# Optimization experiments

Measured on AMD Instinct MI355X. Metric: run time of the kernel, lower is better.

## Reference

```python
import jax, jax.numpy as jnp
import numpy as np
import math

D = 768
H = 12
HD = D // H  # 64


def setup_inputs() -> dict:
    key = jax.random.key(0)
    ks = jax.random.split(key, 8)
    B, S = 32, 127
    desc = jax.random.normal(ks[0], (B, S, D), dtype=jnp.float32)
    nv = jax.random.normal(ks[1], (B, S + 1, D), dtype=jnp.float32)
    def xavier(k, shape):
        fan_in, fan_out = shape[1], shape[0]
        gain = 1.0 / math.sqrt(2.0)
        limit = gain * math.sqrt(6.0 / (fan_in + fan_out))
        return jax.random.uniform(k, shape, jnp.float32, -limit, limit)
    Wq = xavier(ks[2], (D, D)); bq = jnp.zeros((D,), jnp.float32)
    Wk = xavier(ks[3], (D, D)); bk = jnp.zeros((D,), jnp.float32)
    Wv = xavier(ks[4], (D, D)); bv = jnp.zeros((D,), jnp.float32)
    # attn_proj: Linear(3*head_dim, 1)
    Wa = xavier(ks[5], (1, 3 * HD))[0]  # [3*HD]
    ba = jnp.zeros((), jnp.float32)
    return {
        "desc_embeddings": desc,
        "name_value_embeddings": nv,
        "Wq": Wq, "bq": bq, "Wk": Wk, "bk": bk, "Wv": Wv, "bv": bv,
        "Wa": Wa, "ba": ba,
    }


def _forward(desc_embeddings, name_value_embeddings, Wq, bq, Wk, bk, Wv, bv, Wa, ba):
    B, new_seq, _ = name_value_embeddings.shape
    S = new_seq - 1

    # adjacency: var-var all ones, CLS->Var row = 1, Var->CLS col = 0, CLS->CLS = 0
    adj = jnp.zeros((new_seq, new_seq), jnp.float32)
    adj = adj.at[1:, 1:].set(1.0)
    adj = adj.at[0, 1:].set(1.0)
    adj = jnp.broadcast_to(adj, (B, new_seq, new_seq))

    # q,k,v: [B, H, new_seq, HD]
    def proj(W, b):
        y = name_value_embeddings @ W.T + b
        return y.reshape(B, new_seq, H, HD).transpose(0, 2, 1, 3)
    q = proj(Wq, bq); k = proj(Wk, bk); v = proj(Wv, bv)

    # attn_proj weight split: [q_part | k_part | edge_part], each [HD]
    wq_a, wk_a, we_a = Wa[:HD], Wa[HD:2 * HD], Wa[2 * HD:]

    # q/k scalar contributions per (b,h,i) and (b,h,j)
    lq = jnp.einsum('bhid,d->bhi', q, wq_a)  # [B,H,new_seq]
    lk = jnp.einsum('bhjd,d->bhj', k, wk_a)  # [B,H,new_seq]

    # edge_attr[b,i,j] per head h (head slice of concat[node_i_desc, node_j_desc]):
    # edge vector = concat(desc_i, desc_j)[h*HD:(h+1)*HD] viewed as [H, HD] of 2D dims.
    # concat(desc_i, desc_j) has 2D dims -> reshaped to [H, HD] means head h takes
    # slice [h*HD:(h+1)*HD] of the 2D-dim concat. Heads 0..H/2-1 come from desc_i,
    # heads H/2..H-1 come from desc_j. Compute edge dot with we_a accordingly.
    # desc_full[b,t] : [B,S,D]. Build per-head contributions:
    # for h < H//2: edge slice = desc_i[h*HD:(h+1)*HD]  -> depends only on i
    # for h >= H//2: edge slice = desc_j[(h-H//2)*HD:(h-H//2+1)*HD] -> depends only on j
    desc_heads = desc_embeddings.reshape(B, S, H // 2, 2 * HD)  # wrong split; do directly
    # Direct: per head h, slice indices into the 2D concat vector
    dh = desc_embeddings.reshape(B, S, H, HD)  # desc split into H chunks of HD (covers D = H*HD)
    # concat(desc_i,desc_j) reshaped to [H,HD]: heads 0..H/2-1 use dh_i[:, :, h],
    # heads H/2..H-1 use dh_j[:, :, h - H/2]
    e_dot = jnp.einsum('bshd,d->bsh', dh, jnp.broadcast_to(we_a, (HD,)))  # placeholder, recompute per head below
    # per-head edge scalar contribution for var-var edges:
    ei = jnp.einsum('bshd,d->bhs', dh, we_a)  # contribution if head slice comes from desc at position s
    Hh = H // 2
    # var-var logits edge part: for h<Hh depends on i; for h>=Hh depends on j
    le_i = ei[:, :Hh, :]   # [B,Hh,S] depends on i (row)
    le_j = ei[:, Hh:, :]   # [B,Hh,S] depends on j (col)

    # CLS edges: cls_edge_attr = concat(desc, desc) at position t (the var index)
    # row 0 (CLS->var j): edge = concat(desc_j, desc_j) -> head h slice:
    #   h<Hh: dh_j[h]; h>=Hh: dh_j[h-Hh]  -> scalar ei[b,h,j] with h mapped
    e_cls = jnp.concatenate([ei[:, :Hh, :], ei[:, :Hh, :]], axis=1) * 0  # init
    e_cls = jnp.concatenate([le_i, le_i], axis=1)  # [B,H,S]: head h<Hh uses dh[h], h>=Hh uses dh[h-Hh]
    # note ei[:, :Hh] corresponds to dh chunks 0..Hh-1 ; for h>=Hh slice is dh[h-Hh] -> same le_i

    # Assemble full logits [B,H,new_seq,new_seq]
    logits = lq[:, :, :, None] + lk[:, :, None, :]
    # edge contributions (only where adj==1; edge_attr zeroed elsewhere by mask mult)
    edge = jnp.zeros((B, H, new_seq, new_seq), jnp.float32)
    # var-var block [1:,1:]
    ev = jnp.zeros((B, H, S, S), jnp.float32)
    ev = ev + jnp.pad(le_i, ((0, 0), (0, Hh), (0, 0)))[:, :, :, None] * 0  # keep shapes
    ev_i = jnp.concatenate([le_i, jnp.zeros_like(le_j)], axis=1)  # h<Hh: i-dependent
    ev_j = jnp.concatenate([jnp.zeros_like(le_i), le_j], axis=1)  # h>=Hh: j-dependent
    ev = ev_i[:, :, :, None] + ev_j[:, :, None, :]  # [B,H,S,S]
    edge = edge.at[:, :, 1:, 1:].set(ev)
    # CLS row (0, 1:): cls_edge = concat(desc_j,desc_j); j = column var
    edge = edge.at[:, :, 0, 1:].set(e_cls)
    # CLS col (1:, 0): cls_edge = concat(desc_i,desc_i) BUT adj[:,1:,0]=0 so edge_attr
    # multiplied by adj -> zero; also masked out. edge stays 0, but torch zeroes it too.
    # mask edge by adjacency (edge_attr *= adj)
    edge = edge * adj[:, None, :, :]
    logits = logits + edge + ba

    mask = (adj[:, None, :, :] == 0).astype(jnp.float32) * -1e9
    logits = logits + mask
    attn = jax.nn.softmax(logits, axis=-1)  # [B,H,new_seq,new_seq]
    ctx = jnp.einsum('bhij,bhjd->bhid', attn, v)
    basis_outputs = ctx.transpose(0, 2, 1, 3)  # [B,new_seq,H,HD]
    return basis_outputs, attn


def reference(desc_embeddings, name_value_embeddings, Wq, bq, Wk, bk, Wv, bv, Wa, ba):
    return _forward(desc_embeddings, name_value_embeddings, Wq, bq, Wk, bk, Wv, bv, Wa, ba)
```

## Files before the change

kernel.cpp:

```cpp
#include <hip/hip_runtime.h>

#define NB 32
#define NS 128
#define SD 127
#define ND 768
#define NH 12
#define HD 64

__device__ inline float wredSum(float v){
  #pragma unroll
  for (int off=32; off>0; off>>=1) v += __shfl_xor(v, off);
  return v;
}
__device__ inline float wredMax(float v){
  #pragma unroll
  for (int off=32; off>0; off>>=1) v = fmaxf(v, __shfl_xor(v, off));
  return v;
}

__global__ __launch_bounds__(256)
void fold_ei(const float* __restrict__ Wk, const float* __restrict__ bk,
             const float* __restrict__ desc, const float* __restrict__ Wa,
             float* __restrict__ uk, float* __restrict__ bkdot,
             float* __restrict__ ei){
  int blk = blockIdx.x, t = threadIdx.x;
  int wave = t >> 6, lane = t & 63;
  if (blk < 144){
    __shared__ float red[4][64];
    int h = blk/12, cb = blk%12;
    int c0 = t & 63, dg = t >> 6;
    const float* base = Wk + (size_t)(h*HD + dg*16)*ND + cb*64 + c0;
    float acc = 0.f;
    #pragma unroll
    for (int i=0;i<16;++i) acc += base[(size_t)i*ND] * Wa[64 + dg*16 + i];
    red[dg][c0] = acc;
    __syncthreads();
    if (dg==0) uk[h*ND + cb*64 + c0] = red[0][c0]+red[1][c0]+red[2][c0]+red[3][c0];
    if (blk==0 && t < NH){
      float a = 0.f;
      for (int d=0; d<64; ++d) a += bk[t*HD+d]*Wa[64+d];
      bkdot[t] = a;
    }
  } else {
    int bs = blk - 144;
    int b = bs / SD, s = bs % SD;
    float wea = Wa[128 + lane];
    const float* row = desc + (size_t)bs * ND;
    #pragma unroll
    for (int hh=0; hh<3; ++hh){
      int h = wave + hh*4;
      float v = row[h*HD + lane] * wea;
      v = wredSum(v);
      if (lane==0) ei[(size_t)(b*NH + h)*NS + s] = v;
    }
  }
}

__global__ __launch_bounds__(256)
void lk_kernel(const float* __restrict__ nv, const float* __restrict__ uk,
               const float* __restrict__ bkdot, float* __restrict__ lk){
  __shared__ __align__(16) float S[4*ND];
  int blk = blockIdx.x, t = threadIdx.x, wave = t>>6, lane = t&63;
  float ukr[3][12], bkd[3];
  #pragma unroll
  for (int hh=0; hh<3; ++hh){
    int h = wave*3 + hh;
    bkd[hh] = bkdot[h];
    #pragma unroll
    for (int k=0;k<12;++k) ukr[hh][k] = uk[h*ND + lane + 64*k];
  }
  int j0 = blk*4;
  const float4* src = (const float4*)(nv + (size_t)j0*ND);
  ((float4*)S)[t]     = src[t];
  ((float4*)S)[t+256] = src[t+256];
  ((float4*)S)[t+512] = src[t+512];
  __syncthreads();
  float acc[12];
  #pragma unroll
  for (int rr=0; rr<4; ++rr)
    #pragma unroll
    for (int hh=0; hh<3; ++hh){
      float a = 0.f;
      #pragma unroll
      for (int k=0;k<12;++k) a += S[rr*ND + lane + 64*k]*ukr[hh][k];
      acc[rr*3+hh] = a;
    }
  #pragma unroll
  for (int i=0;i<12;++i) acc[i] = wredSum(acc[i]);
  if (lane == 0){
    int b = j0 >> 7, jb = j0 & 127;
    #pragma unroll
    for (int rr=0; rr<4; ++rr)
      #pragma unroll
      for (int hh=0; hh<3; ++hh)
        lk[(size_t)(b*NH + wave*3 + hh)*NS + jb + rr] = acc[rr*3+hh] + bkd[hh];
  }
}

__global__ __launch_bounds__(256)
void msoft_attn(const float* __restrict__ nv, const float* __restrict__ lk,
                const float* __restrict__ ei, float* __restrict__ m_part,
                float* __restrict__ out){
  int blk = blockIdx.x;
  int b = blk >> 4, jg = blk & 15;
  int t = threadIdx.x, wave = t >> 6, lane = t & 63;
  __shared__ float slk[NH*NS];
  __shared__ float sei[NH*NS];
  __shared__ float wf[24][NS];
  for (int i=t; i<NH*NS; i+=256) slk[i] = lk[(size_t)b*NH*NS + i];
  for (int i=t; i<NH*NS; i+=256) sei[i] = ei[(size_t)b*NH*NS + i];
  __syncthreads();
  #pragma unroll
  for (int rr=0; rr<6; ++rr){
    int r = wave*6 + rr;
    int h = r >> 1, which = r & 1;
    const float* eirow = (which==0) ? (sei + (h%6)*NS) : (sei + h*NS);
    float g = (which==0) ? 1.f : (h>=6 ? 1.f : 0.f);
    float x0 = (lane>=1) ? slk[h*NS+lane] + g*eirow[lane-1] : -3.0e38f;
    float x1 = slk[h*NS+lane+64] + g*eirow[lane+63];
    float mm = wredMax(fmaxf(x0,x1));
    float e0 = (lane>=1) ? __expf(x0-mm) : 0.f;
    float e1 = __expf(x1-mm);
    float s  = wredSum(e0+e1);
    float inv = 1.f/s;
    wf[r][lane]    = e0*inv;
    wf[r][lane+64] = e1*inv;
  }
  __syncthreads();
  if (t < 192){
    const float4* nvb = (const float4*)(nv + ((size_t)b*NS + jg*8)*ND);
    float4 acc[24];
    #pragma unroll
    for (int r=0;r<24;++r) acc[r] = make_float4(0.f,0.f,0.f,0.f);
    #pragma unroll
    for (int jj=0; jj<8; ++jj){
      float4 x = nvb[jj*192 + t];
      int j = jg*8 + jj;
      #pragma unroll
      for (int r=0;r<24;++r){
        float wr = wf[r][j];
        acc[r].x += wr*x.x; acc[r].y += wr*x.y;
        acc[r].z += wr*x.z; acc[r].w += wr*x.w;
      }
    }
    #pragma unroll
    for (int r=0;r<24;++r)
      ((float4*)(m_part + ((size_t)(b*24 + r)*16 + jg)*ND))[t] = acc[r];
  }
  float* abase = out + (size_t)NB*NS*ND + (size_t)(b*NH)*NS*NS;
  for (int idx=t; idx<3072; idx+=256){
    int h = idx >> 8;
    int rem = idx & 255;
    int il = rem >> 5, q = rem & 31;
    int i = jg*8 + il;
    const float* srcw = (i==0) ? wf[h*2] : wf[h*2+1];
    float4 v = { srcw[q*4], srcw[q*4+1], srcw[q*4+2], srcw[q*4+3] };
    ((float4*)(abase + (size_t)h*NS*NS))[i*32 + q] = v;
  }
}

__global__ __launch_bounds__(256)
void proj_basis(const float* __restrict__ m_part, const float* __restrict__ Wv,
                const float* __restrict__ bv, float* __restrict__ out){
  int bh = blockIdx.x;
  int b = bh / NH, h = bh % NH;
  int t = threadIdx.x, wave = t >> 6, lane = t & 63;
  __shared__ __align__(16) float msum[2*ND];
  __shared__ float cvec[2*HD];
  for (int i=t; i<384; i+=256){
    int rl = (i >= 192);
    int c4 = i - rl*192;
    const float4* mp = (const float4*)(m_part + ((size_t)(b*24 + h*2 + rl)*16)*ND) + c4;
    float4 s = make_float4(0.f,0.f,0.f,0.f);
    #pragma unroll
    for (int g=0; g<16; ++g){
      float4 v = mp[g*192];
      s.x += v.x; s.y += v.y; s.z += v.z; s.w += v.w;
    }
    ((float4*)msum)[i] = s;
  }
  __syncthreads();
  #pragma unroll
  for (int dd=0; dd<16; ++dd){
    int d = wave*16 + dd;
    const float* wvr = Wv + (size_t)(h*HD + d)*ND;
    float p0=0.f, p1=0.f;
    #pragma unroll
    for (int k=0; k<12; ++k){
      float wv = wvr[lane + 64*k];
      p0 += wv*msum[lane + 64*k];
      p1 += wv*msum[ND + lane + 64*k];
    }
    p0 = wredSum(p0); p1 = wredSum(p1);
    if (lane==0){
      float bb = bv[h*HD + d];
      cvec[d]    = p0 + bb;
      cvec[64+d] = p1 + bb;
    }
  }
  __syncthreads();
  float* bo = out + (size_t)b*NS*ND + h*HD;
  #pragma unroll
  for (int k=0;k<8;++k){
    int idx = t + k*256;
    int i = idx>>4, q = idx&15;
    const float* srcc = (i==0) ? cvec : cvec+64;
    float4 v = { srcc[q*4], srcc[q*4+1], srcc[q*4+2], srcc[q*4+3] };
    *(float4*)(bo + (size_t)i*ND + q*4) = v;
  }
}

extern "C" void kernel_launch(void* const* d_in, const int* in_sizes, int n_in,
                              void* d_out, int out_size, void* d_ws, size_t ws_size,
                              hipStream_t stream) {
  const float* desc = (const float*)d_in[0];
  const float* nv   = (const float*)d_in[1];
  const float* Wk   = (const float*)d_in[4];
  const float* bk   = (const float*)d_in[5];
  const float* Wv   = (const float*)d_in[6];
  const float* bv   = (const float*)d_in[7];
  const float* Wa   = (const float*)d_in[8];
  float* out = (float*)d_out;
  float* ws  = (float*)d_ws;

  float* uk     = ws;
  float* bkdot  = ws + 9216;
  float* eibuf  = ws + 9232;
  float* lkbuf  = ws + 58384;
  float* m_part = ws + 107536;

  fold_ei   <<<4208, 256, 0, stream>>>(Wk, bk, desc, Wa, uk, bkdot, eibuf);
  lk_kernel <<<1024, 256, 0, stream>>>(nv, uk, bkdot, lkbuf);
  msoft_attn<<<512,  256, 0, stream>>>(nv, lkbuf, eibuf, m_part, out);
  proj_basis<<<384,  256, 0, stream>>>(m_part, Wv, bv, out);
}
```

Before: 140.2 us.

## Fuse softmax-weighted sum and Wv projection into one per-(batch,head) kernel

Merges msoft_attn and proj_basis into a single kernel with one block per (batch, head). Each block computes its two softmax rows, reduces nv over all positions into shared memory, writes the attention map, then projects through the head's Wv slice. This removes the m_part partial-sum buffer round trip and one launch. Block order is swizzled so concurrent blocks share a batch's nv in cache. The cost is that each block streams the full nv batch (128x768 floats) using only 192 threads, so per-block serial work and nv re-reads across heads go up.

```diff
diff --git a/kernel.cpp b/kernel.cpp
--- a/kernel.cpp
+++ b/kernel.cpp
@@ -98,115 +98,98 @@
 }
 
 __global__ __launch_bounds__(256)
-void msoft_attn(const float* __restrict__ nv, const float* __restrict__ lk,
-                const float* __restrict__ ei, float* __restrict__ m_part,
-                float* __restrict__ out){
-  int blk = blockIdx.x;
-  int b = blk >> 4, jg = blk & 15;
+void attn_fused(const float* __restrict__ nv, const float* __restrict__ lk,
+                const float* __restrict__ ei, const float* __restrict__ Wv,
+                const float* __restrict__ bv, float* __restrict__ out){
+  int logical = ((blockIdx.x & 7) * 48) + (blockIdx.x >> 3);
+  int b = logical / NH, h = logical % NH;
   int t = threadIdx.x, wave = t >> 6, lane = t & 63;
-  __shared__ float slk[NH*NS];
-  __shared__ float sei[NH*NS];
-  __shared__ float wf[24][NS];
-  for (int i=t; i<NH*NS; i+=256) slk[i] = lk[(size_t)b*NH*NS + i];
-  for (int i=t; i<NH*NS; i+=256) sei[i] = ei[(size_t)b*NH*NS + i];
-  __syncthreads();
-  #pragma unroll
-  for (int rr=0; rr<6; ++rr){
-    int r = wave*6 + rr;
-    int h = r >> 1, which = r & 1;
-    const float* eirow = (which==0) ? (sei + (h%6)*NS) : (sei + h*NS);
-    float g = (which==0) ? 1.f : (h>=6 ? 1.f : 0.f);
-    float x0 = (lane>=1) ? slk[h*NS+lane] + g*eirow[lane-1] : -3.0e38f;
-    float x1 = slk[h*NS+lane+64] + g*eirow[lane+63];
+  __shared__ __align__(16) float slk[NS];
+  __shared__ __align__(16) float sei0[NS];
+  __shared__ __align__(16) float sei1[NS];
+  __shared__ __align__(16) float wf0[NS];
+  __shared__ __align__(16) float wf1[NS];
+  __shared__ __align__(16) float msum0[ND];
+  __shared__ __align__(16) float msum1[ND];
+  __shared__ __align__(16) float cvec0[HD];
+  __shared__ __align__(16) float cvec1[HD];
+
+  if (t < NS) slk[t] = lk[(size_t)(b*NH + h)*NS + t];
+  if (t < SD) sei0[t] = ei[(size_t)(b*NH + (h % 6))*NS + t];
+  if (t >= 128 && t < 128 + SD) sei1[t-128] = ei[(size_t)(b*NH + h)*NS + (t-128)];
+  __syncthreads();
+
+  if (wave < 2){
+    const float* eir = (wave==0) ? sei0 : sei1;
+    float g = (wave==0) ? 1.f : (h >= 6 ? 1.f : 0.f);
+    float x0 = (lane>=1) ? slk[lane] + g*eir[lane-1] : -3.0e38f;
+    float x1 = slk[lane+64] + g*eir[lane+63];
     float mm = wredMax(fmaxf(x0,x1));
     float e0 = (lane>=1) ? __expf(x0-mm) : 0.f;
     float e1 = __expf(x1-mm);
     float s  = wredSum(e0+e1);
     float inv = 1.f/s;
-    wf[r][lane]    = e0*inv;
-    wf[r][lane+64] = e1*inv;
-  }
-  __syncthreads();
-  if (t < 192){
-    const float4* nvb = (const float4*)(nv + ((size_t)b*NS + jg*8)*ND);
-    float4 acc[24];
-    #pragma unroll
-    for (int r=0;r<24;++r) acc[r] = make_float4(0.f,0.f,0.f,0.f);
-    #pragma unroll
-    for (int jj=0; jj<8; ++jj){
-      float4 x = nvb[jj*192 + t];
-      int j = jg*8 + jj;
-      #pragma unroll
-      for (int r=0;r<24;++r){
-        float wr = wf[r][j];
-        acc[r].x += wr*x.x; acc[r].y += wr*x.y;
-        acc[r].z += wr*x.z; acc[r].w += wr*x.w;
-      }
-    }
-    #pragma unroll
-    for (int r=0;r<24;++r)
-      ((float4*)(m_part + ((size_t)(b*24 + r)*16 + jg)*ND))[t] = acc[r];
-  }
-  float* abase = out + (size_t)NB*NS*ND + (size_t)(b*NH)*NS*NS;
-  for (int idx=t; idx<3072; idx+=256){
-    int h = idx >> 8;
-    int rem = idx & 255;
-    int il = rem >> 5, q = rem & 31;
-    int i = jg*8 + il;
-    const float* srcw = (i==0) ? wf[h*2] : wf[h*2+1];
-    float4 v = { srcw[q*4], srcw[q*4+1], srcw[q*4+2], srcw[q*4+3] };
-    ((float4*)(abase + (size_t)h*NS*NS))[i*32 + q] = v;
-  }
-}
-
-__global__ __launch_bounds__(256)
-void proj_basis(const float* __restrict__ m_part, const float* __restrict__ Wv,
-                const float* __restrict__ bv, float* __restrict__ out){
-  int bh = blockIdx.x;
-  int b = bh / NH, h = bh % NH;
-  int t = threadIdx.x, wave = t >> 6, lane = t & 63;
-  __shared__ __align__(16) float msum[2*ND];
-  __shared__ float cvec[2*HD];
-  for (int i=t; i<384; i+=256){
-    int rl = (i >= 192);
-    int c4 = i - rl*192;
-    const float4* mp = (const float4*)(m_part + ((size_t)(b*24 + h*2 + rl)*16)*ND) + c4;
-    float4 s = make_float4(0.f,0.f,0.f,0.f);
-    #pragma unroll
-    for (int g=0; g<16; ++g){
-      float4 v = mp[g*192];
-      s.x += v.x; s.y += v.y; s.z += v.z; s.w += v.w;
-    }
-    ((float4*)msum)[i] = s;
-  }
-  __syncthreads();
+    float* wf = (wave==0) ? wf0 : wf1;
+    wf[lane]    = e0*inv;
+    wf[lane+64] = e1*inv;
+  }
+  __syncthreads();
+
+  if (wave < 3){
+    const float4* nvb = (const float4*)(nv + (size_t)b*NS*ND);
+    float4 a0 = make_float4(0.f,0.f,0.f,0.f);
+    float4 a1 = make_float4(0.f,0.f,0.f,0.f);
+    #pragma unroll 4
+    for (int j=1; j<NS; ++j){
+      float4 x = nvb[(size_t)j*192 + t];
+      float w0 = wf0[j], w1 = wf1[j];
+      a0.x += w0*x.x; a0.y += w0*x.y; a0.z += w0*x.z; a0.w += w0*x.w;
+      a1.x += w1*x.x; a1.y += w1*x.y; a1.z += w1*x.z; a1.w += w1*x.w;
+    }
+    ((float4*)msum0)[t] = a0;
+    ((float4*)msum1)[t] = a1;
+  } else {
+    float4* abase = (float4*)(out + (size_t)NB*NS*ND + (size_t)(b*NH + h)*NS*NS);
+    const float4* w0v = (const float4*)wf0;
+    const float4* w1v = (const float4*)wf1;
+    #pragma unroll
+    for (int k=0; k<64; ++k){
+      int idx = lane + k*64;
+      int q = idx & 31;
+      abase[idx] = (idx < 32) ? w0v[q] : w1v[q];
+    }
+  }
+  __syncthreads();
+
+  const float* wvh = Wv + (size_t)h*HD*ND;
   #pragma unroll
   for (int dd=0; dd<16; ++dd){
     int d = wave*16 + dd;
-    const float* wvr = Wv + (size_t)(h*HD + d)*ND;
+    const float* wvr = wvh + (size_t)d*ND;
     float p0=0.f, p1=0.f;
     #pragma unroll
     for (int k=0; k<12; ++k){
       float wv = wvr[lane + 64*k];
-      p0 += wv*msum[lane + 64*k];
-      p1 += wv*msum[ND + lane + 64*k];
+      p0 += wv*msum0[lane + 64*k];
+      p1 += wv*msum1[lane + 64*k];
     }
     p0 = wredSum(p0); p1 = wredSum(p1);
     if (lane==0){
       float bb = bv[h*HD + d];
-      cvec[d]    = p0 + bb;
-      cvec[64+d] = p1 + bb;
-    }
-  }
-  __syncthreads();
+      cvec0[d] = p0 + bb;
+      cvec1[d] = p1 + bb;
+    }
+  }
+  __syncthreads();
+
   float* bo = out + (size_t)b*NS*ND + h*HD;
-  #pragma unroll
-  for (int k=0;k<8;++k){
+  const float4* c0 = (const float4*)cvec0;
+  const float4* c1 = (const float4*)cvec1;
+  #pragma unroll
+  for (int k=0; k<8; ++k){
     int idx = t + k*256;
-    int i = idx>>4, q = idx&15;
-    const float* srcc = (i==0) ? cvec : cvec+64;
-    float4 v = { srcc[q*4], srcc[q*4+1], srcc[q*4+2], srcc[q*4+3] };
-    *(float4*)(bo + (size_t)i*ND + q*4) = v;
+    int i = idx >> 4, q = idx & 15;
+    *(float4*)(bo + (size_t)i*ND + q*4) = (i==0) ? c0[q] : c1[q];
   }
 }
 
@@ -227,10 +210,8 @@
   float* bkdot  = ws + 9216;
   float* eibuf  = ws + 9232;
   float* lkbuf  = ws + 58384;
-  float* m_part = ws + 107536;
 
   fold_ei   <<<4208, 256, 0, stream>>>(Wk, bk, desc, Wa, uk, bkdot, eibuf);
   lk_kernel <<<1024, 256, 0, stream>>>(nv, uk, bkdot, lkbuf);
-  msoft_attn<<<512,  256, 0, stream>>>(nv, lkbuf, eibuf, m_part, out);
-  proj_basis<<<384,  256, 0, stream>>>(m_part, Wv, bv, out);
-}
+  attn_fused<<<384,  256, 0, stream>>>(nv, lkbuf, eibuf, Wv, bv, out);
+}
```

Result: faster. 136.8 us (-2.4%).
